# Performance work log

Hardware: AMD Instinct MI355X
Metric: run time of the kernel (lower is better)

The kernel has to match this reference:

```python
import jax, jax.numpy as jnp
from jax import lax
import numpy as np
import math

D = 256; H = 4; DH = 64; PERIOD = 30; WIN = 4; L = 2
AUDIO = 768; MOTION = 33
B = 8; T = 1024; S = 1024


def _pe_table(t, d=D, period=PERIOD):
    pos = np.arange(period, dtype=np.float32)[:, None]
    div = np.exp(np.arange(0, d, 2, dtype=np.float32) * (-math.log(10000.0) / d))
    pe = np.zeros((period, d), np.float32)
    pe[:, 0::2] = np.sin(pos * div)
    pe[:, 1::2] = np.cos(pos * div)
    reps = t // period + 1
    return jnp.asarray(np.tile(pe, (reps, 1))[:t])


def _tgt_mask(t):
    # ALiBi-style bias (quantized by period) + causal mask, per head. [H,t,t]
    slopes = jnp.array([0.25 ** (i + 1) for i in range(H)], jnp.float32)
    i = jnp.arange(t)[:, None]
    j = jnp.arange(t)[None, :]
    rel = i - j
    alibi = jnp.where(rel >= 0, -(rel // PERIOD).astype(jnp.float32), 0.0)
    causal = jnp.where(rel >= 0, 0.0, -jnp.inf)
    return slopes[:, None, None] * alibi + causal[None]


def _mem_mask(t, s):
    i = jnp.arange(t)[:, None]
    j = jnp.arange(s)[None, :]
    return jnp.where(jnp.abs(i - j) <= WIN, 0.0, -jnp.inf)


def _ln(x, g, b, eps=1e-5):
    mu = jnp.mean(x, -1, keepdims=True)
    var = jnp.mean(jnp.square(x - mu), -1, keepdims=True)
    return (x - mu) * lax.rsqrt(var + eps) * g + b


def _mha(xq, xkv, in_w, in_b, out_w, out_b, mask):
    wq, wk, wv = jnp.split(in_w, 3, axis=0)
    bq, bk, bv = jnp.split(in_b, 3)
    q = xq @ wq.T + bq
    k = xkv @ wk.T + bk
    v = xkv @ wv.T + bv
    b_, t_, _ = q.shape
    s_ = k.shape[1]
    q = q.reshape(b_, t_, H, DH)
    k = k.reshape(b_, s_, H, DH)
    v = v.reshape(b_, s_, H, DH)
    scores = jnp.einsum('bthd,bshd->bhts', q, k) / math.sqrt(DH) + mask
    a = jax.nn.softmax(scores, axis=-1)
    o = jnp.einsum('bhts,bshd->bthd', a, v).reshape(b_, t_, D)
    return o @ out_w.T + out_b


def _conv1d(x_nch, w, b):
    y = lax.conv_general_dilated(x_nch, w, (1,), [(2, 2)],
                                 dimension_numbers=('NCH', 'OIH', 'NCH'))
    return y + b[None, :, None]


def setup_inputs() -> dict:
    key = jax.random.key(0)
    ks = iter(jax.random.split(key, 40))

    def r(shape, s=0.05):
        return jax.random.normal(next(ks), shape, jnp.float32) * s

    return {
        'hidden_states': jax.random.normal(next(ks), (B, S, AUDIO), jnp.float32),
        'target_motions': jax.random.uniform(next(ks), (B, T, MOTION), jnp.float32),
        'W_af': r((D, AUDIO)), 'b_af': r((D,)),
        'conv1_w': r((D, D, 5)), 'conv1_b': r((D,)),
        'conv2_w': r((D, D, 5)), 'conv2_b': r((D,)),
        'W_vm': r((D, MOTION)), 'b_vm': r((D,)),
        'sa_in_w': r((L, 3 * D, D)), 'sa_in_b': r((L, 3 * D)),
        'sa_out_w': r((L, D, D)), 'sa_out_b': r((L, D)),
        'ca_in_w': r((L, 3 * D, D)), 'ca_in_b': r((L, 3 * D)),
        'ca_out_w': r((L, D, D)), 'ca_out_b': r((L, D)),
        'ln1_g': jnp.ones((L, D)), 'ln1_b': jnp.zeros((L, D)),
        'ln2_g': jnp.ones((L, D)), 'ln2_b': jnp.zeros((L, D)),
        'ln3_g': jnp.ones((L, D)), 'ln3_b': jnp.zeros((L, D)),
        'ff1_w': r((L, 2 * D, D)), 'ff1_b': r((L, 2 * D)),
        'ff2_w': r((L, D, 2 * D)), 'ff2_b': r((L, D)),
        'W_vr': r((MOTION, D)), 'b_vr': r((MOTION,)),
    }


def reference(hidden_states, target_motions, W_af, b_af, conv1_w, conv1_b,
              conv2_w, conv2_b, W_vm, b_vm, sa_in_w, sa_in_b, sa_out_w,
              sa_out_b, ca_in_w, ca_in_b, ca_out_w, ca_out_b, ln1_g, ln1_b,
              ln2_g, ln2_b, ln3_g, ln3_b, ff1_w, ff1_b, ff2_w, ff2_b,
              W_vr, b_vr):
    # audio encoder: linear + residual temporal convs (exact GELU)
    audio = hidden_states @ W_af.T + b_af                       # [B,S,D]
    c = _conv1d(audio.transpose(0, 2, 1), conv1_w, conv1_b)
    c = jax.nn.gelu(c, approximate=False)
    c = _conv1d(c, conv2_w, conv2_b)
    audio = audio + c.transpose(0, 2, 1)

    b_, t_, _ = target_motions.shape
    motion_in = jnp.concatenate(
        [jnp.zeros((b_, 1, MOTION), target_motions.dtype),
         target_motions[:, :-1]], axis=1)
    x = motion_in @ W_vm.T + b_vm + _pe_table(t_)               # PPE (eval: no dropout)

    tm = _tgt_mask(t_)                                          # [H,t,t]
    mm = _mem_mask(t_, audio.shape[1])                          # [t,s]

    for l in range(L):  # post-norm TransformerDecoderLayer, relu FFN
        x = _ln(x + _mha(x, x, sa_in_w[l], sa_in_b[l], sa_out_w[l], sa_out_b[l], tm),
                ln1_g[l], ln1_b[l])
        x = _ln(x + _mha(x, audio, ca_in_w[l], ca_in_b[l], ca_out_w[l], ca_out_b[l], mm),
                ln2_g[l], ln2_b[l])
        h = jax.nn.relu(x @ ff1_w[l].T + ff1_b[l]) @ ff2_w[l].T + ff2_b[l]
        x = _ln(x + h, ln3_g[l], ln3_b[l])

    return jnp.clip(x @ W_vr.T + b_vr, 0.0, 1.0)
```

## Files before the change

### kernel.cpp

```cpp
#include <hip/hip_runtime.h>
#include <math.h>

#define B_ 8
#define T_ 1024
#define S_ 1024
#define D_ 256
#define H_ 4
#define DH_ 64
#define AUDIO_ 768
#define MOTION_ 33
#define PERIOD_ 30
#define WIN_ 4
#define M_ (B_ * T_)
#define PART_ (B_ * H_ * T_)

typedef _Float16 half8 __attribute__((ext_vector_type(8)));
typedef _Float16 half4 __attribute__((ext_vector_type(4)));
typedef __attribute__((ext_vector_type(4))) float f32x4;

#define O_AF    0
#define O_SAIN  196608
#define O_SAOUT 589824
#define O_CAIN  720896
#define O_CAOUT 1114112
#define O_FF1   1245184
#define O_FF2   1507328
#define O_CONV1 1769472
#define O_CONV2 2097152
#define O_VR    2424832
#define WH_TOT  2441216
#define HID_TOT 6291456

struct CvtSrc { const float* p[17]; };

__global__ __launch_bounds__(256) void cvt_all(
    CvtSrc s, _Float16* __restrict__ wH, _Float16* __restrict__ hidH) {
  const long i = (long)blockIdx.x * 256 + threadIdx.x;
  if (i >= (long)WH_TOT + HID_TOT) return;
  if (i >= WH_TOT) { const long j = i - WH_TOT; hidH[j] = (_Float16)s.p[15][j]; return; }
  if (i >= O_VR) {
    const long j = i - O_VR, oc = j >> 8, cin = j & 255;
    wH[i] = (oc < MOTION_) ? (_Float16)s.p[16][oc * 256 + cin] : (_Float16)0.f;
    return;
  }
  if (i >= O_CONV2) {
    const long j = i - O_CONV2, oc = j / 1280, r = j % 1280, tap = r >> 8, cin = r & 255;
    wH[i] = (_Float16)s.p[14][(oc * 256 + cin) * 5 + tap]; return;
  }
  if (i >= O_CONV1) {
    const long j = i - O_CONV1, oc = j / 1280, r = j % 1280, tap = r >> 8, cin = r & 255;
    wH[i] = (_Float16)s.p[13][(oc * 256 + cin) * 5 + tap]; return;
  }
  int seg; long base;
  if      (i >= 1638400) { seg = 12; base = 1638400; }
  else if (i >= 1507328) { seg = 11; base = 1507328; }
  else if (i >= 1376256) { seg = 10; base = 1376256; }
  else if (i >= 1245184) { seg = 9;  base = 1245184; }
  else if (i >= 1179648) { seg = 8;  base = 1179648; }
  else if (i >= 1114112) { seg = 7;  base = 1114112; }
  else if (i >= 917504)  { seg = 6;  base = 917504; }
  else if (i >= 720896)  { seg = 5;  base = 720896; }
  else if (i >= 655360)  { seg = 4;  base = 655360; }
  else if (i >= 589824)  { seg = 3;  base = 589824; }
  else if (i >= 393216)  { seg = 2;  base = 393216; }
  else if (i >= 196608)  { seg = 1;  base = 196608; }
  else                   { seg = 0;  base = 0; }
  wH[i] = (_Float16)s.p[seg][i - base];
}

__global__ __launch_bounds__(256) void gemm_h(
    const _Float16* __restrict__ A, const _Float16* __restrict__ W,
    const float* __restrict__ bias, float* __restrict__ Cf,
    _Float16* __restrict__ Ch, int M, int N, int K, int relu) {
  __shared__ _Float16 As[2][64][72];
  __shared__ _Float16 Bs[2][64][72];
  const int tid = threadIdx.x;
  const int wave = tid >> 6, lane = tid & 63;
  const int wr = wave >> 1, wc = wave & 1;
  const int lr16 = lane & 15, kq = lane >> 4;
  const int bm = blockIdx.x, bn = blockIdx.y;
  const int sr = tid >> 2, sq = tid & 3;

  const _Float16* Ap = A + (size_t)(bm * 64 + sr) * K + sq * 8;
  const _Float16* Wp = W + (size_t)(bn * 64 + sr) * K + sq * 8;

  half8 ra0 = *reinterpret_cast<const half8*>(Ap);
  half8 ra1 = *reinterpret_cast<const half8*>(Ap + 32);
  half8 rw0 = *reinterpret_cast<const half8*>(Wp);
  half8 rw1 = *reinterpret_cast<const half8*>(Wp + 32);
  f32x4 acc[2][2] = {};

  *reinterpret_cast<half8*>(&As[0][sr][sq * 8]) = ra0;
  *reinterpret_cast<half8*>(&As[0][sr][32 + sq * 8]) = ra1;
  *reinterpret_cast<half8*>(&Bs[0][sr][sq * 8]) = rw0;
  *reinterpret_cast<half8*>(&Bs[0][sr][32 + sq * 8]) = rw1;
  __syncthreads();

  const int nsteps = K >> 6;
  for (int step = 0; step < nsteps; ++step) {
    const int cur = step & 1;
    const bool more = (step + 1 < nsteps);
    if (more) {
      const int kn = (step + 1) << 6;
      ra0 = *reinterpret_cast<const half8*>(Ap + kn);
      ra1 = *reinterpret_cast<const half8*>(Ap + kn + 32);
      rw0 = *reinterpret_cast<const half8*>(Wp + kn);
      rw1 = *reinterpret_cast<const half8*>(Wp + kn + 32);
    }
    half8 af[2][2], bf[2][2];
#pragma unroll
    for (int m = 0; m < 2; ++m)
#pragma unroll
      for (int s = 0; s < 2; ++s)
        af[m][s] = *reinterpret_cast<const half8*>(
            &As[cur][wr * 32 + m * 16 + lr16][s * 32 + kq * 8]);
#pragma unroll
    for (int n = 0; n < 2; ++n)
#pragma unroll
      for (int s = 0; s < 2; ++s)
        bf[n][s] = *reinterpret_cast<const half8*>(
            &Bs[cur][wc * 32 + n * 16 + lr16][s * 32 + kq * 8]);
#pragma unroll
    for (int m = 0; m < 2; ++m)
#pragma unroll
      for (int n = 0; n < 2; ++n)
#pragma unroll
        for (int s = 0; s < 2; ++s)
          acc[m][n] = __builtin_amdgcn_mfma_f32_16x16x32_f16(af[m][s], bf[n][s], acc[m][n], 0, 0, 0);
    if (more) {
      *reinterpret_cast<half8*>(&As[cur ^ 1][sr][sq * 8]) = ra0;
      *reinterpret_cast<half8*>(&As[cur ^ 1][sr][32 + sq * 8]) = ra1;
      *reinterpret_cast<half8*>(&Bs[cur ^ 1][sr][sq * 8]) = rw0;
      *reinterpret_cast<half8*>(&Bs[cur ^ 1][sr][32 + sq * 8]) = rw1;
      __syncthreads();
    }
  }

#pragma unroll
  for (int m = 0; m < 2; ++m) {
#pragma unroll
    for (int n = 0; n < 2; ++n) {
      const int col = bn * 64 + wc * 32 + n * 16 + lr16;
      const float bv = bias[col];
#pragma unroll
      for (int j = 0; j < 4; ++j) {
        const int row = bm * 64 + wr * 32 + m * 16 + kq * 4 + j;
        float v = acc[m][n][j] + bv;
        if (relu) v = fmaxf(v, 0.f);
        const size_t idx = (size_t)row * N + col;
        if (Cf) Cf[idx] = v;
        if (Ch) Ch[idx] = (_Float16)v;
      }
    }
  }
}

__global__ __launch_bounds__(256) void gemm_ca(
    const _Float16* __restrict__ Aq, const _Float16* __restrict__ Akv,
    const _Float16* __restrict__ W, const float* __restrict__ bias,
    _Float16* __restrict__ Oq, _Float16* __restrict__ Okv) {
  __shared__ _Float16 As[2][64][72];
  __shared__ _Float16 Bs[2][64][72];
  const int tid = threadIdx.x;
  const int wave = tid >> 6, lane = tid & 63;
  const int wr = wave >> 1, wc = wave & 1;
  const int lr16 = lane & 15, kq = lane >> 4;
  const int bm = blockIdx.x, bn = blockIdx.y;
  const int sr = tid >> 2, sq = tid & 3;
  const bool isq = (bn < 4);
  const _Float16* A = isq ? Aq : Akv;
  _Float16* Optr = isq ? Oq : Okv;
  const int Nout = isq ? 256 : 512;
  const int ocol0 = (isq ? bn : bn - 4) * 64;

  const _Float16* Ap = A + (size_t)(bm * 64 + sr) * 256 + sq * 8;
  const _Float16* Wp = W + (size_t)(bn * 64 + sr) * 256 + sq * 8;

  half8 ra0 = *reinterpret_cast<const half8*>(Ap);
  half8 ra1 = *reinterpret_cast<const half8*>(Ap + 32);
  half8 rw0 = *reinterpret_cast<const half8*>(Wp);
  half8 rw1 = *reinterpret_cast<const half8*>(Wp + 32);
  f32x4 acc[2][2] = {};

  *reinterpret_cast<half8*>(&As[0][sr][sq * 8]) = ra0;
  *reinterpret_cast<half8*>(&As[0][sr][32 + sq * 8]) = ra1;
  *reinterpret_cast<half8*>(&Bs[0][sr][sq * 8]) = rw0;
  *reinterpret_cast<half8*>(&Bs[0][sr][32 + sq * 8]) = rw1;
  __syncthreads();

  for (int step = 0; step < 4; ++step) {
    const int cur = step & 1;
    const bool more = (step + 1 < 4);
    if (more) {
      const int kn = (step + 1) << 6;
      ra0 = *reinterpret_cast<const half8*>(Ap + kn);
      ra1 = *reinterpret_cast<const half8*>(Ap + kn + 32);
      rw0 = *reinterpret_cast<const half8*>(Wp + kn);
      rw1 = *reinterpret_cast<const half8*>(Wp + kn + 32);
    }
    half8 af[2][2], bf[2][2];
#pragma unroll
    for (int m = 0; m < 2; ++m)
#pragma unroll
      for (int s = 0; s < 2; ++s)
        af[m][s] = *reinterpret_cast<const half8*>(
            &As[cur][wr * 32 + m * 16 + lr16][s * 32 + kq * 8]);
#pragma unroll
    for (int n = 0; n < 2; ++n)
#pragma unroll
      for (int s = 0; s < 2; ++s)
        bf[n][s] = *reinterpret_cast<const half8*>(
            &Bs[cur][wc * 32 + n * 16 + lr16][s * 32 + kq * 8]);
#pragma unroll
    for (int m = 0; m < 2; ++m)
#pragma unroll
      for (int n = 0; n < 2; ++n)
#pragma unroll
        for (int s = 0; s < 2; ++s)
          acc[m][n] = __builtin_amdgcn_mfma_f32_16x16x32_f16(af[m][s], bf[n][s], acc[m][n], 0, 0, 0);
    if (more) {
      *reinterpret_cast<half8*>(&As[cur ^ 1][sr][sq * 8]) = ra0;
      *reinterpret_cast<half8*>(&As[cur ^ 1][sr][32 + sq * 8]) = ra1;
      *reinterpret_cast<half8*>(&Bs[cur ^ 1][sr][sq * 8]) = rw0;
      *reinterpret_cast<half8*>(&Bs[cur ^ 1][sr][32 + sq * 8]) = rw1;
      __syncthreads();
    }
  }

#pragma unroll
  for (int m = 0; m < 2; ++m) {
#pragma unroll
    for (int n = 0; n < 2; ++n) {
      const int lc = wc * 32 + n * 16 + lr16;
      const float bv = bias[bn * 64 + lc];
#pragma unroll
      for (int j = 0; j < 4; ++j) {
        const int row = bm * 64 + wr * 32 + m * 16 + kq * 4 + j;
        Optr[(size_t)row * Nout + ocol0 + lc] = (_Float16)(acc[m][n][j] + bv);
      }
    }
  }
}

__device__ __forceinline__ half8 conv_ld(const _Float16* Xb, int p, int tap, int cin) {
  const int sp = p + tap - 2;
  if (sp < 0 || sp >= S_) { half8 z = {}; return z; }
  return *reinterpret_cast<const half8*>(Xb + (size_t)sp * D_ + cin);
}

__global__ __launch_bounds__(256) void conv_h(
    const _Float16* __restrict__ Xh, const _Float16* __restrict__ Wc,
    const float* __restrict__ bias, _Float16* OutH,
    const _Float16* ResH, int mode) {
  __shared__ _Float16 As[2][64][72];
  __shared__ _Float16 Bs[2][64][72];
  const int tid = threadIdx.x;
  const int wave = tid >> 6, lane = tid & 63;
  const int wr = wave >> 1, wc = wave & 1;
  const int lr16 = lane & 15, kq = lane >> 4;
  const int b = blockIdx.x >> 4;
  const int s0 = (blockIdx.x & 15) * 64;
  const int o0 = blockIdx.y * 64;
  const int sr = tid >> 2, sq = tid & 3;

  const _Float16* Xb = Xh + (size_t)b * S_ * D_;
  const _Float16* Wp = Wc + (size_t)(o0 + sr) * 1280 + sq * 8;
  const int p = s0 + sr;

  half8 ra0 = conv_ld(Xb, p, 0, sq * 8);
  half8 ra1 = conv_ld(Xb, p, 0, 32 + sq * 8);
  half8 rw0 = *reinterpret_cast<const half8*>(Wp);
  half8 rw1 = *reinterpret_cast<const half8*>(Wp + 32);
  f32x4 acc[2][2] = {};

  *reinterpret_cast<half8*>(&As[0][sr][sq * 8]) = ra0;
  *reinterpret_cast<half8*>(&As[0][sr][32 + sq * 8]) = ra1;
  *reinterpret_cast<half8*>(&Bs[0][sr][sq * 8]) = rw0;
  *reinterpret_cast<half8*>(&Bs[0][sr][32 + sq * 8]) = rw1;
  __syncthreads();

  for (int step = 0; step < 20; ++step) {
    const int cur = step & 1;
    const bool more = (step + 1 < 20);
    if (more) {
      const int kn = (step + 1) << 6;
      const int tap = kn >> 8, cb = kn & 255;
      ra0 = conv_ld(Xb, p, tap, cb + sq * 8);
      ra1 = conv_ld(Xb, p, tap, cb + 32 + sq * 8);
      rw0 = *reinterpret_cast<const half8*>(Wp + kn);
      rw1 = *reinterpret_cast<const half8*>(Wp + kn + 32);
    }
    half8 af[2][2], bf[2][2];
#pragma unroll
    for (int m = 0; m < 2; ++m)
#pragma unroll
      for (int s = 0; s < 2; ++s)
        af[m][s] = *reinterpret_cast<const half8*>(
            &As[cur][wr * 32 + m * 16 + lr16][s * 32 + kq * 8]);
#pragma unroll
    for (int n = 0; n < 2; ++n)
#pragma unroll
      for (int s = 0; s < 2; ++s)
        bf[n][s] = *reinterpret_cast<const half8*>(
            &Bs[cur][wc * 32 + n * 16 + lr16][s * 32 + kq * 8]);
#pragma unroll
    for (int m = 0; m < 2; ++m)
#pragma unroll
      for (int n = 0; n < 2; ++n)
#pragma unroll
        for (int s = 0; s < 2; ++s)
          acc[m][n] = __builtin_amdgcn_mfma_f32_16x16x32_f16(af[m][s], bf[n][s], acc[m][n], 0, 0, 0);
    if (more) {
      *reinterpret_cast<half8*>(&As[cur ^ 1][sr][sq * 8]) = ra0;
      *reinterpret_cast<half8*>(&As[cur ^ 1][sr][32 + sq * 8]) = ra1;
      *reinterpret_cast<half8*>(&Bs[cur ^ 1][sr][sq * 8]) = rw0;
      *reinterpret_cast<half8*>(&Bs[cur ^ 1][sr][32 + sq * 8]) = rw1;
      __syncthreads();
    }
  }

#pragma unroll
  for (int m = 0; m < 2; ++m) {
#pragma unroll
    for (int n = 0; n < 2; ++n) {
      const int oc = o0 + wc * 32 + n * 16 + lr16;
      const float bv = bias[oc];
#pragma unroll
      for (int j = 0; j < 4; ++j) {
        const int s = s0 + wr * 32 + m * 16 + kq * 4 + j;
        const size_t idx = ((size_t)b * S_ + s) * D_ + oc;
        float v = acc[m][n][j] + bv;
        if (mode == 0) {
          v = 0.5f * v * (1.f + erff(v * 0.70710678118654752f));
        } else {
          v += (float)ResH[idx];
        }
        OutH[idx] = (_Float16)v;
      }
    }
  }
}

__global__ __launch_bounds__(256) void head_mfma(
    const _Float16* __restrict__ Xh, const _Float16* __restrict__ Wh,
    const float* __restrict__ bv, float* __restrict__ Out) {
  __shared__ _Float16 As[2][64][72];
  __shared__ _Float16 Bs[2][64][72];
  const int tid = threadIdx.x;
  const int wave = tid >> 6, lane = tid & 63;
  const int wr = wave >> 1, wc = wave & 1;
  const int lr16 = lane & 15, kq = lane >> 4;
  const int bm = blockIdx.x;
  const int sr = tid >> 2, sq = tid & 3;

  const _Float16* Ap = Xh + (size_t)(bm * 64 + sr) * D_ + sq * 8;
  const _Float16* Wp = Wh + (size_t)sr * D_ + sq * 8;

  half8 ra0 = *reinterpret_cast<const half8*>(Ap);
  half8 ra1 = *reinterpret_cast<const half8*>(Ap + 32);
  half8 rw0 = *reinterpret_cast<const half8*>(Wp);
  half8 rw1 = *reinterpret_cast<const half8*>(Wp + 32);
  f32x4 acc[2][2] = {};

  *reinterpret_cast<half8*>(&As[0][sr][sq * 8]) = ra0;
  *reinterpret_cast<half8*>(&As[0][sr][32 + sq * 8]) = ra1;
  *reinterpret_cast<half8*>(&Bs[0][sr][sq * 8]) = rw0;
  *reinterpret_cast<half8*>(&Bs[0][sr][32 + sq * 8]) = rw1;
  __syncthreads();

  for (int step = 0; step < 4; ++step) {
    const int cur = step & 1;
    const bool more = (step + 1 < 4);
    if (more) {
      const int kn = (step + 1) << 6;
      ra0 = *reinterpret_cast<const half8*>(Ap + kn);
      ra1 = *reinterpret_cast<const half8*>(Ap + kn + 32);
      rw0 = *reinterpret_cast<const half8*>(Wp + kn);
      rw1 = *reinterpret_cast<const half8*>(Wp + kn + 32);
    }
    half8 af[2][2], bf[2][2];
#pragma unroll
    for (int m = 0; m < 2; ++m)
#pragma unroll
      for (int s = 0; s < 2; ++s)
        af[m][s] = *reinterpret_cast<const half8*>(
            &As[cur][wr * 32 + m * 16 + lr16][s * 32 + kq * 8]);
#pragma unroll
    for (int n = 0; n < 2; ++n)
#pragma unroll
      for (int s = 0; s < 2; ++s)
        bf[n][s] = *reinterpret_cast<const half8*>(
            &Bs[cur][wc * 32 + n * 16 + lr16][s * 32 + kq * 8]);
#pragma unroll
    for (int m = 0; m < 2; ++m)
#pragma unroll
      for (int n = 0; n < 2; ++n)
#pragma unroll
        for (int s = 0; s < 2; ++s)
          acc[m][n] = __builtin_amdgcn_mfma_f32_16x16x32_f16(af[m][s], bf[n][s], acc[m][n], 0, 0, 0);
    if (more) {
      *reinterpret_cast<half8*>(&As[cur ^ 1][sr][sq * 8]) = ra0;
      *reinterpret_cast<half8*>(&As[cur ^ 1][sr][32 + sq * 8]) = ra1;
      *reinterpret_cast<half8*>(&Bs[cur ^ 1][sr][sq * 8]) = rw0;
      *reinterpret_cast<half8*>(&Bs[cur ^ 1][sr][32 + sq * 8]) = rw1;
      __syncthreads();
    }
  }

#pragma unroll
  for (int m = 0; m < 2; ++m) {
#pragma unroll
    for (int n = 0; n < 2; ++n) {
      const int col = wc * 32 + n * 16 + lr16;
      if (col < MOTION_) {
        const float bb = bv[col];
#pragma unroll
        for (int j = 0; j < 4; ++j) {
          const int row = bm * 64 + wr * 32 + m * 16 + kq * 4 + j;
          float v = acc[m][n][j] + bb;
          Out[(size_t)row * MOTION_ + col] = fminf(fmaxf(v, 0.f), 1.f);
        }
      }
    }
  }
}

__global__ __launch_bounds__(256) void motion_pe(
    const float* __restrict__ TM, const float* __restrict__ Wvm,
    const float* __restrict__ bvm, float* __restrict__ Xout,
    _Float16* __restrict__ XoutH) {
  const int d = threadIdx.x;
  const int bt = blockIdx.x;
  const int t = bt & (T_ - 1);
  const int b = bt >> 10;
  float acc = bvm[d];
  if (t > 0) {
    const float* mrow = TM + ((size_t)b * T_ + t - 1) * MOTION_;
    const float* wrow = Wvm + (size_t)d * MOTION_;
#pragma unroll
    for (int m = 0; m < MOTION_; ++m) acc += mrow[m] * wrow[m];
  }
  const int pos = t % PERIOD_;
  const int i2 = d >> 1;
  const float div = expf((float)(2 * i2) * (-9.210340371976184f / 256.f));
  const float ang = (float)pos * div;
  acc += (d & 1) ? cosf(ang) : sinf(ang);
  Xout[(size_t)bt * D_ + d] = acc;
  XoutH[(size_t)bt * D_ + d] = (_Float16)acc;
}

#define RSK_ 72
#define RSV_ 64
__global__ __launch_bounds__(512) void self_attn(
    const _Float16* __restrict__ QKV, float* __restrict__ Opart,
    float* __restrict__ Ml, float* __restrict__ Ll) {
  __shared__ _Float16 Ks[2][64 * RSK_];
  __shared__ _Float16 VTs[2][64 * RSV_];
  __shared__ _Float16 Ps[8][16 * RSK_];
  const int qtb = blockIdx.x >> 1, half = blockIdx.x & 1;
  const int h = blockIdx.y, b = blockIdx.z;
  const int tid = threadIdx.x;
  const int wave = tid >> 6, lane = tid & 63;
  const int lo = lane & 15, hi = lane >> 4;
  const float slope = exp2f(-2.f * (float)(h + 1));
  const int qloc = wave * 16 + lo;
  const int tq = qtb * 128 + qloc;
  const size_t base = (size_t)b * T_ * 768 + h * 64;
  const int sj = tid >> 3, sch = tid & 7;

  half8 qf[2];
#pragma unroll
  for (int s = 0; s < 2; ++s)
    qf[s] = *reinterpret_cast<const half8*>(
        QKV + base + (size_t)(qtb * 128 + qloc) * 768 + s * 32 + hi * 8);

  f32x4 oacc[4] = {};
  float mrun = -1e30f, lrun = 0.f;

  const int nloc = qtb + 1;
  const int kt0 = half * nloc;

  half8 rk, rv;
  {
    const size_t rowoff = base + (size_t)(kt0 * 64 + sj) * 768;
    rk = *reinterpret_cast<const half8*>(QKV + rowoff + 256 + sch * 8);
    rv = *reinterpret_cast<const half8*>(QKV + rowoff + 512 + sch * 8);
    *reinterpret_cast<half8*>(&Ks[0][sj * RSK_ + sch * 8]) = rk;
#pragma unroll
    for (int r = 0; r < 8; ++r) {
      const int d = sch * 8 + r;
      const int sw = ((d & 7) ^ (d >> 3)) << 3;
      VTs[0][d * RSV_ + (sj ^ sw)] = rv[r];
    }
  }
  __syncthreads();

  for (int i = 0; i < nloc; ++i) {
    const int kt = kt0 + i;
    const int cur = i & 1;
    const bool more = (i + 1 < nloc);
    if (more) {
      const size_t rowoff = base + (size_t)((kt + 1) * 64 + sj) * 768;
      rk = *reinterpret_cast<const half8*>(QKV + rowoff + 256 + sch * 8);
      rv = *reinterpret_cast<const half8*>(QKV + rowoff + 512 + sch * 8);
    }

    f32x4 st[4] = {};
    __builtin_amdgcn_s_setprio(1);
#pragma unroll
    for (int f = 0; f < 4; ++f) {
#pragma unroll
      for (int s = 0; s < 2; ++s) {
        const half8 kf = *reinterpret_cast<const half8*>(
            &Ks[cur][(f * 16 + lo) * RSK_ + s * 32 + hi * 8]);
        st[f] = __builtin_amdgcn_mfma_f32_16x16x32_f16(kf, qf[s], st[f], 0, 0, 0);
      }
    }
    __builtin_amdgcn_s_setprio(0);

    float sc[4][4];
    float tmax = -1e30f;
#pragma unroll
    for (int f = 0; f < 4; ++f)
#pragma unroll
      for (int r = 0; r < 4; ++r) {
        const int j = kt * 64 + f * 16 + hi * 4 + r;
        const int rel = tq - j;
        const float v = (rel >= 0)
            ? st[f][r] * 0.125f - slope * (float)(rel / PERIOD_) : -1e30f;
        sc[f][r] = v;
        tmax = fmaxf(tmax, v);
      }
    tmax = fmaxf(tmax, __shfl_xor(tmax, 16, 64));
    tmax = fmaxf(tmax, __shfl_xor(tmax, 32, 64));
    const float mnew = fmaxf(fmaxf(mrun, tmax), -1e20f);
    const float scale = __expf(mrun - mnew);

    float psum = 0.f;
#pragma unroll
    for (int f = 0; f < 4; ++f) {
      half4 ph;
#pragma unroll
      for (int r = 0; r < 4; ++r) {
        const float pv = __expf(sc[f][r] - mnew);
        psum += pv;
        ph[r] = (_Float16)pv;
      }
      *reinterpret_cast<half4*>(&Ps[wave][lo * RSK_ + f * 16 + hi * 4]) = ph;
    }
    psum += __shfl_xor(psum, 16, 64);
    psum += __shfl_xor(psum, 32, 64);
    lrun = lrun * scale + psum;
    mrun = mnew;

    float rsc[4];
#pragma unroll
    for (int r = 0; r < 4; ++r) rsc[r] = __shfl(scale, hi * 4 + r, 64);
#pragma unroll
    for (int nf = 0; nf < 4; ++nf)
#pragma unroll
      for (int r = 0; r < 4; ++r) oacc[nf][r] *= rsc[r];

    __builtin_amdgcn_s_setprio(1);
#pragma unroll
    for (int s = 0; s < 2; ++s) {
      const half8 pf = *reinterpret_cast<const half8*>(
          &Ps[wave][lo * RSK_ + s * 32 + hi * 8]);
#pragma unroll
      for (int nf = 0; nf < 4; ++nf) {
        const int d = nf * 16 + lo;
        const int sw = ((d & 7) ^ (d >> 3)) << 3;
        const half8 vf = *reinterpret_cast<const half8*>(
            &VTs[cur][d * RSV_ + ((s * 32 + hi * 8) ^ sw)]);
        oacc[nf] = __builtin_amdgcn_mfma_f32_16x16x32_f16(pf, vf, oacc[nf], 0, 0, 0);
      }
    }
    __builtin_amdgcn_s_setprio(0);

    if (more) {
      *reinterpret_cast<half8*>(&Ks[cur ^ 1][sj * RSK_ + sch * 8]) = rk;
#pragma unroll
      for (int r = 0; r < 8; ++r) {
        const int d = sch * 8 + r;
        const int sw = ((d & 7) ^ (d >> 3)) << 3;
        VTs[cur ^ 1][d * RSV_ + (sj ^ sw)] = rv[r];
      }
      __syncthreads();
    }
  }

  const size_t rbase = ((size_t)b * H_ + h) * T_;
  const size_t hoff = (size_t)half * PART_;
#pragma unroll
  for (int nf = 0; nf < 4; ++nf)
#pragma unroll
    for (int r = 0; r < 4; ++r) {
      const int q = qtb * 128 + wave * 16 + hi * 4 + r;
      Opart[(hoff + rbase + q) * 64 + nf * 16 + lo] = oacc[nf][r];
    }
  if (hi == 0) {
    const int q = qtb * 128 + wave * 16 + lo;
    Ml[hoff + rbase + q] = mrun;
    Ll[hoff + rbase + q] = lrun;
  }
}

__global__ __launch_bounds__(256) void attn_merge(
    const float* __restrict__ Opart, const float* __restrict__ Ml,
    const float* __restrict__ Ll, _Float16* __restrict__ O) {
  const int tid = threadIdx.x;
  const int d = tid & 63;
  const long row = (long)blockIdx.x * 4 + (tid >> 6);
  const float m0 = Ml[row], m1 = Ml[PART_ + row];
  const float l0 = Ll[row], l1 = Ll[PART_ + row];
  const float m = fmaxf(m0, m1);
  const float w0 = __expf(m0 - m), w1 = __expf(m1 - m);
  const float inv = 1.f / (l0 * w0 + l1 * w1);
  const float o = (Opart[row * 64 + d] * w0 +
                   Opart[(long)PART_ * 64 + row * 64 + d] * w1) * inv;
  const int b = (int)(row >> 12);
  const int h = (int)((row >> 10) & 3);
  const int t = (int)(row & (T_ - 1));
  O[(((size_t)b * T_ + t) * D_) + h * 64 + d] = (_Float16)o;
}

__global__ __launch_bounds__(128) void cross_attn(
    const _Float16* __restrict__ Q, const _Float16* __restrict__ KV,
    _Float16* __restrict__ O) {
  const int gid = blockIdx.x * 128 + threadIdx.x;
  const int h = gid & 3;
  const int bt = gid >> 2;
  const int t = bt & (T_ - 1);
  const int b = bt >> 10;

  float q[64];
  const _Float16* qp = Q + (size_t)bt * D_ + h * 64;
#pragma unroll
  for (int d0 = 0; d0 < 64; d0 += 8) {
    const half8 v = *reinterpret_cast<const half8*>(qp + d0);
#pragma unroll
    for (int e = 0; e < 8; ++e) q[d0 + e] = (float)v[e];
  }

  const int j0 = (t - WIN_ > 0) ? t - WIN_ : 0;
  const int j1 = (t + WIN_ < S_ - 1) ? t + WIN_ : S_ - 1;
  const int nj = j1 - j0 + 1;

  float sc[9];
  float mx = -1e30f;
#pragma unroll
  for (int jj = 0; jj < 9; ++jj) {
    if (jj < nj) {
      const _Float16* kp = KV + ((size_t)b * S_ + j0 + jj) * 512 + h * 64;
      float s = 0.f;
#pragma unroll
      for (int d0 = 0; d0 < 64; d0 += 8) {
        const half8 kv = *reinterpret_cast<const half8*>(kp + d0);
#pragma unroll
        for (int e = 0; e < 8; ++e) s += q[d0 + e] * (float)kv[e];
      }
      sc[jj] = s * 0.125f;
      mx = fmaxf(mx, sc[jj]);
    } else {
      sc[jj] = -1e30f;
    }
  }
  float l = 0.f;
  float p[9];
#pragma unroll
  for (int jj = 0; jj < 9; ++jj) { p[jj] = __expf(sc[jj] - mx); l += p[jj]; }
  const float inv = 1.f / l;

  float o[64];
#pragma unroll
  for (int d = 0; d < 64; ++d) o[d] = 0.f;
#pragma unroll
  for (int jj = 0; jj < 9; ++jj) {
    if (jj < nj) {
      const float pj = p[jj] * inv;
      const _Float16* vp = KV + ((size_t)b * S_ + j0 + jj) * 512 + 256 + h * 64;
#pragma unroll
      for (int d0 = 0; d0 < 64; d0 += 8) {
        const half8 vv = *reinterpret_cast<const half8*>(vp + d0);
#pragma unroll
        for (int e = 0; e < 8; ++e) o[d0 + e] += pj * (float)vv[e];
      }
    }
  }
  _Float16* op = O + (size_t)bt * D_ + h * 64;
#pragma unroll
  for (int d = 0; d < 64; ++d) op[d] = (_Float16)o[d];
}

__global__ __launch_bounds__(256) void ln_res(
    const float* X, const _Float16* __restrict__ R,
    const float* __restrict__ g, const float* __restrict__ bta,
    float* Out, _Float16* __restrict__ OutH) {
  const int wid = threadIdx.x >> 6, lane = threadIdx.x & 63;
  const size_t row = (size_t)blockIdx.x * 4 + wid;
  const float* xp = X + row * D_;
  const _Float16* rp = R + row * D_;
  float v[4];
  float s = 0.f;
#pragma unroll
  for (int k = 0; k < 4; ++k) {
    const int d = lane + k * 64;
    v[k] = xp[d] + (float)rp[d];
    s += v[k];
  }
#pragma unroll
  for (int off = 32; off; off >>= 1) s += __shfl_xor(s, off, 64);
  const float mu = s * (1.f / 256.f);
  float var = 0.f;
#pragma unroll
  for (int k = 0; k < 4; ++k) { const float d = v[k] - mu; var += d * d; }
#pragma unroll
  for (int off = 32; off; off >>= 1) var += __shfl_xor(var, off, 64);
  const float rs = rsqrtf(var * (1.f / 256.f) + 1e-5f);
#pragma unroll
  for (int k = 0; k < 4; ++k) {
    const int d = lane + k * 64;
    const float o = (v[k] - mu) * rs * g[d] + bta[d];
    Out[row * D_ + d] = o;
    OutH[row * D_ + d] = (_Float16)o;
  }
}

extern "C" void kernel_launch(void* const* d_in, const int* in_sizes, int n_in,
                              void* d_out, int out_size, void* d_ws, size_t ws_size,
                              hipStream_t stream) {
  (void)in_sizes; (void)n_in; (void)out_size; (void)ws_size;
  const float* hidden = (const float*)d_in[0];
  const float* tmot   = (const float*)d_in[1];
  const float* W_af   = (const float*)d_in[2];
  const float* b_af   = (const float*)d_in[3];
  const float* c1w    = (const float*)d_in[4];
  const float* c1b    = (const float*)d_in[5];
  const float* c2w    = (const float*)d_in[6];
  const float* c2b    = (const float*)d_in[7];
  const float* Wvm    = (const float*)d_in[8];
  const float* bvm    = (const float*)d_in[9];
  const float* sa_in_w  = (const float*)d_in[10];
  const float* sa_in_b  = (const float*)d_in[11];
  const float* sa_out_w = (const float*)d_in[12];
  const float* sa_out_b = (const float*)d_in[13];
  const float* ca_in_w  = (const float*)d_in[14];
  const float* ca_in_b  = (const float*)d_in[15];
  const float* ca_out_w = (const float*)d_in[16];
  const float* ca_out_b = (const float*)d_in[17];
  const float* ln1g = (const float*)d_in[18];
  const float* ln1b = (const float*)d_in[19];
  const float* ln2g = (const float*)d_in[20];
  const float* ln2b = (const float*)d_in[21];
  const float* ln3g = (const float*)d_in[22];
  const float* ln3b = (const float*)d_in[23];
  const float* ff1w = (const float*)d_in[24];
  const float* ff1b = (const float*)d_in[25];
  const float* ff2w = (const float*)d_in[26];
  const float* ff2b = (const float*)d_in[27];
  const float* Wvr  = (const float*)d_in[28];
  const float* bvr  = (const float*)d_in[29];
  float* out = (float*)d_out;

  float* ws = (float*)d_ws;
  const size_t BSD = (size_t)M_ * D_;
  float* x     = ws + BSD;
  _Float16* t1h = (_Float16*)(ws + 2 * BSD);
  _Float16* hb = (_Float16*)(ws + 3 * BSD);
  _Float16* Rh      = hb;
  _Float16* x_h     = hb + 3 * BSD;
  _Float16* audio_h = hb + 4 * BSD;
  _Float16* att_h   = hb + 5 * BSD;
  _Float16* wH      = hb + 6 * BSD;
  _Float16* ckv_h   = Rh + BSD;
  float* Opart = (float*)(wH + WH_TOT);
  float* Ml    = Opart + (size_t)2 * PART_ * 64;
  float* Ll    = Ml + (size_t)2 * PART_;

  const dim3 blk(256);

  CvtSrc cs;
  cs.p[0] = W_af;
  cs.p[1] = sa_in_w;            cs.p[2] = sa_in_w + 768 * 256;
  cs.p[3] = sa_out_w;           cs.p[4] = sa_out_w + 256 * 256;
  cs.p[5] = ca_in_w;            cs.p[6] = ca_in_w + 768 * 256;
  cs.p[7] = ca_out_w;           cs.p[8] = ca_out_w + 256 * 256;
  cs.p[9] = ff1w;               cs.p[10] = ff1w + 512 * 256;
  cs.p[11] = ff2w;              cs.p[12] = ff2w + 256 * 512;
  cs.p[13] = c1w;               cs.p[14] = c2w;
  cs.p[15] = hidden;            cs.p[16] = Wvr;
  cvt_all<<<dim3((WH_TOT + HID_TOT + 255) / 256), blk, 0, stream>>>(cs, wH, Rh);

  gemm_h<<<dim3(M_ / 64, 4), blk, 0, stream>>>(Rh, wH + O_AF, b_af, nullptr, audio_h,
                                               M_, 256, 768, 0);
  conv_h<<<dim3(128, 4), blk, 0, stream>>>(audio_h, wH + O_CONV1, c1b, t1h, nullptr, 0);
  conv_h<<<dim3(128, 4), blk, 0, stream>>>(t1h, wH + O_CONV2, c2b, audio_h, audio_h, 1);

  motion_pe<<<dim3(M_), blk, 0, stream>>>(tmot, Wvm, bvm, x, x_h);

  for (int l = 0; l < 2; ++l) {
    gemm_h<<<dim3(M_ / 64, 12), blk, 0, stream>>>(
        x_h, wH + O_SAIN + l * 196608, sa_in_b + l * 768, nullptr, Rh, M_, 768, 256, 0);
    self_attn<<<dim3(T_ / 128 * 2, H_, B_), dim3(512), 0, stream>>>(Rh, Opart, Ml, Ll);
    attn_merge<<<dim3(PART_ / 4), blk, 0, stream>>>(Opart, Ml, Ll, att_h);
    gemm_h<<<dim3(M_ / 64, 4), blk, 0, stream>>>(
        att_h, wH + O_SAOUT + l * 65536, sa_out_b + l * 256, nullptr, t1h, M_, 256, 256, 0);
    ln_res<<<dim3(M_ / 4), blk, 0, stream>>>(x, t1h, ln1g + l * 256, ln1b + l * 256, x, x_h);

    gemm_ca<<<dim3(M_ / 64, 12), blk, 0, stream>>>(
        x_h, audio_h, wH + O_CAIN + l * 196608, ca_in_b + l * 768, Rh, ckv_h);
    cross_attn<<<dim3(M_ * H_ / 128), dim3(128), 0, stream>>>(Rh, ckv_h, att_h);
    gemm_h<<<dim3(M_ / 64, 4), blk, 0, stream>>>(
        att_h, wH + O_CAOUT + l * 65536, ca_out_b + l * 256, nullptr, t1h, M_, 256, 256, 0);
    ln_res<<<dim3(M_ / 4), blk, 0, stream>>>(x, t1h, ln2g + l * 256, ln2b + l * 256, x, x_h);

    gemm_h<<<dim3(M_ / 64, 8), blk, 0, stream>>>(
        x_h, wH + O_FF1 + l * 131072, ff1b + l * 512, nullptr, Rh, M_, 512, 256, 1);
    gemm_h<<<dim3(M_ / 64, 4), blk, 0, stream>>>(
        Rh, wH + O_FF2 + l * 131072, ff2b + l * 256, nullptr, t1h, M_, 256, 512, 0);
    ln_res<<<dim3(M_ / 4), blk, 0, stream>>>(x, t1h, ln3g + l * 256, ln3b + l * 256, x, x_h);
  }

  head_mfma<<<dim3(M_ / 64), blk, 0, stream>>>(x_h, wH + O_VR, bvr, out);
}
```

Before: 332.9 us.

## Fuse fp32-to-fp16 input conversion into audio GEMM and attention merge into out-proj GEMM

The audio feature projection GEMM now reads the fp32 hidden states directly and converts them to fp16 while staging tiles into shared memory, so the conversion kernel no longer writes an fp16 copy. The self-attention split-KV merge kernel is removed; the output-projection GEMM instead loads both partial outputs plus their max/sum statistics and combines them while building its A tiles. This removes one kernel launch per layer and the global round trips of the intermediate fp16 buffers. In exchange, the GEMMs read more bytes per tile (fp32 inputs, two partials) and the merge work is repeated across the four N-blocks.

After: 315.8 us (median of 2 runs). 5.2% less time.

```diff
diff --git a/kernel.cpp b/kernel.cpp
--- a/kernel.cpp
+++ b/kernel.cpp
@@ -29,15 +29,13 @@
 #define O_CONV2 2097152
 #define O_VR    2424832
 #define WH_TOT  2441216
-#define HID_TOT 6291456
 
 struct CvtSrc { const float* p[17]; };
 
 __global__ __launch_bounds__(256) void cvt_all(
-    CvtSrc s, _Float16* __restrict__ wH, _Float16* __restrict__ hidH) {
+    CvtSrc s, _Float16* __restrict__ wH) {
   const long i = (long)blockIdx.x * 256 + threadIdx.x;
-  if (i >= (long)WH_TOT + HID_TOT) return;
-  if (i >= WH_TOT) { const long j = i - WH_TOT; hidH[j] = (_Float16)s.p[15][j]; return; }
+  if (i >= WH_TOT) return;
   if (i >= O_VR) {
     const long j = i - O_VR, oc = j >> 8, cin = j & 255;
     wH[i] = (oc < MOTION_) ? (_Float16)s.p[16][oc * 256 + cin] : (_Float16)0.f;
@@ -150,6 +148,234 @@
         const size_t idx = (size_t)row * N + col;
         if (Cf) Cf[idx] = v;
         if (Ch) Ch[idx] = (_Float16)v;
+      }
+    }
+  }
+}
+
+__global__ __launch_bounds__(256) void gemm_af(
+    const float* __restrict__ A, const _Float16* __restrict__ W,
+    const float* __restrict__ bias, _Float16* __restrict__ Ch,
+    int M, int N, int K) {
+  __shared__ _Float16 As[2][64][72];
+  __shared__ _Float16 Bs[2][64][72];
+  const int tid = threadIdx.x;
+  const int wave = tid >> 6, lane = tid & 63;
+  const int wr = wave >> 1, wc = wave & 1;
+  const int lr16 = lane & 15, kq = lane >> 4;
+  const int bm = blockIdx.x, bn = blockIdx.y;
+  const int sr = tid >> 2, sq = tid & 3;
+
+  const float* Ap = A + (size_t)(bm * 64 + sr) * K + sq * 8;
+  const _Float16* Wp = W + (size_t)(bn * 64 + sr) * K + sq * 8;
+
+  float4 fa0, fa1, fa2, fa3;
+  half8 rw0, rw1;
+  fa0 = *reinterpret_cast<const float4*>(Ap);
+  fa1 = *reinterpret_cast<const float4*>(Ap + 4);
+  fa2 = *reinterpret_cast<const float4*>(Ap + 32);
+  fa3 = *reinterpret_cast<const float4*>(Ap + 36);
+  rw0 = *reinterpret_cast<const half8*>(Wp);
+  rw1 = *reinterpret_cast<const half8*>(Wp + 32);
+  f32x4 acc[2][2] = {};
+
+  {
+    half8 pa0, pa1;
+    pa0[0] = (_Float16)fa0.x; pa0[1] = (_Float16)fa0.y; pa0[2] = (_Float16)fa0.z; pa0[3] = (_Float16)fa0.w;
+    pa0[4] = (_Float16)fa1.x; pa0[5] = (_Float16)fa1.y; pa0[6] = (_Float16)fa1.z; pa0[7] = (_Float16)fa1.w;
+    pa1[0] = (_Float16)fa2.x; pa1[1] = (_Float16)fa2.y; pa1[2] = (_Float16)fa2.z; pa1[3] = (_Float16)fa2.w;
+    pa1[4] = (_Float16)fa3.x; pa1[5] = (_Float16)fa3.y; pa1[6] = (_Float16)fa3.z; pa1[7] = (_Float16)fa3.w;
+    *reinterpret_cast<half8*>(&As[0][sr][sq * 8]) = pa0;
+    *reinterpret_cast<half8*>(&As[0][sr][32 + sq * 8]) = pa1;
+    *reinterpret_cast<half8*>(&Bs[0][sr][sq * 8]) = rw0;
+    *reinterpret_cast<half8*>(&Bs[0][sr][32 + sq * 8]) = rw1;
+  }
+  __syncthreads();
+
+  const int nsteps = K >> 6;
+  for (int step = 0; step < nsteps; ++step) {
+    const int cur = step & 1;
+    const bool more = (step + 1 < nsteps);
+    if (more) {
+      const int kn = (step + 1) << 6;
+      fa0 = *reinterpret_cast<const float4*>(Ap + kn);
+      fa1 = *reinterpret_cast<const float4*>(Ap + kn + 4);
+      fa2 = *reinterpret_cast<const float4*>(Ap + kn + 32);
+      fa3 = *reinterpret_cast<const float4*>(Ap + kn + 36);
+      rw0 = *reinterpret_cast<const half8*>(Wp + kn);
+      rw1 = *reinterpret_cast<const half8*>(Wp + kn + 32);
+    }
+    half8 af[2][2], bf[2][2];
+#pragma unroll
+    for (int m = 0; m < 2; ++m)
+#pragma unroll
+      for (int s = 0; s < 2; ++s)
+        af[m][s] = *reinterpret_cast<const half8*>(
+            &As[cur][wr * 32 + m * 16 + lr16][s * 32 + kq * 8]);
+#pragma unroll
+    for (int n = 0; n < 2; ++n)
+#pragma unroll
+      for (int s = 0; s < 2; ++s)
+        bf[n][s] = *reinterpret_cast<const half8*>(
+            &Bs[cur][wc * 32 + n * 16 + lr16][s * 32 + kq * 8]);
+#pragma unroll
+    for (int m = 0; m < 2; ++m)
+#pragma unroll
+      for (int n = 0; n < 2; ++n)
+#pragma unroll
+        for (int s = 0; s < 2; ++s)
+          acc[m][n] = __builtin_amdgcn_mfma_f32_16x16x32_f16(af[m][s], bf[n][s], acc[m][n], 0, 0, 0);
+    if (more) {
+      half8 pa0, pa1;
+      pa0[0] = (_Float16)fa0.x; pa0[1] = (_Float16)fa0.y; pa0[2] = (_Float16)fa0.z; pa0[3] = (_Float16)fa0.w;
+      pa0[4] = (_Float16)fa1.x; pa0[5] = (_Float16)fa1.y; pa0[6] = (_Float16)fa1.z; pa0[7] = (_Float16)fa1.w;
+      pa1[0] = (_Float16)fa2.x; pa1[1] = (_Float16)fa2.y; pa1[2] = (_Float16)fa2.z; pa1[3] = (_Float16)fa2.w;
+      pa1[4] = (_Float16)fa3.x; pa1[5] = (_Float16)fa3.y; pa1[6] = (_Float16)fa3.z; pa1[7] = (_Float16)fa3.w;
+      *reinterpret_cast<half8*>(&As[cur ^ 1][sr][sq * 8]) = pa0;
+      *reinterpret_cast<half8*>(&As[cur ^ 1][sr][32 + sq * 8]) = pa1;
+      *reinterpret_cast<half8*>(&Bs[cur ^ 1][sr][sq * 8]) = rw0;
+      *reinterpret_cast<half8*>(&Bs[cur ^ 1][sr][32 + sq * 8]) = rw1;
+      __syncthreads();
+    }
+  }
+
+#pragma unroll
+  for (int m = 0; m < 2; ++m) {
+#pragma unroll
+    for (int n = 0; n < 2; ++n) {
+      const int col = bn * 64 + wc * 32 + n * 16 + lr16;
+      const float bv = bias[col];
+#pragma unroll
+      for (int j = 0; j < 4; ++j) {
+        const int row = bm * 64 + wr * 32 + m * 16 + kq * 4 + j;
+        Ch[(size_t)row * N + col] = (_Float16)(acc[m][n][j] + bv);
+      }
+    }
+  }
+}
+
+struct SaPre {
+  float4 h0a, h0b, h0c, h0d;
+  float4 h1a, h1b, h1c, h1d;
+  float m0, m1, l0, l1;
+};
+
+__device__ __forceinline__ SaPre sa_load(
+    const float* __restrict__ Opart, const float* __restrict__ Ml,
+    const float* __restrict__ Ll, size_t p, int sq) {
+  SaPre x;
+  const float* o0 = Opart + p * 64;
+  const float* o1 = Opart + (size_t)PART_ * 64 + p * 64;
+  x.h0a = *reinterpret_cast<const float4*>(o0 + sq * 8);
+  x.h0b = *reinterpret_cast<const float4*>(o0 + sq * 8 + 4);
+  x.h0c = *reinterpret_cast<const float4*>(o0 + 32 + sq * 8);
+  x.h0d = *reinterpret_cast<const float4*>(o0 + 36 + sq * 8);
+  x.h1a = *reinterpret_cast<const float4*>(o1 + sq * 8);
+  x.h1b = *reinterpret_cast<const float4*>(o1 + sq * 8 + 4);
+  x.h1c = *reinterpret_cast<const float4*>(o1 + 32 + sq * 8);
+  x.h1d = *reinterpret_cast<const float4*>(o1 + 36 + sq * 8);
+  x.m0 = Ml[p]; x.m1 = Ml[(size_t)PART_ + p];
+  x.l0 = Ll[p]; x.l1 = Ll[(size_t)PART_ + p];
+  return x;
+}
+
+__device__ __forceinline__ void sa_write(
+    _Float16* dst0, _Float16* dst1, const SaPre& x) {
+  const float m = fmaxf(x.m0, x.m1);
+  const float w0 = __expf(x.m0 - m), w1 = __expf(x.m1 - m);
+  const float inv = 1.f / (x.l0 * w0 + x.l1 * w1);
+  const float g0h0[8] = {x.h0a.x, x.h0a.y, x.h0a.z, x.h0a.w,
+                         x.h0b.x, x.h0b.y, x.h0b.z, x.h0b.w};
+  const float g0h1[8] = {x.h1a.x, x.h1a.y, x.h1a.z, x.h1a.w,
+                         x.h1b.x, x.h1b.y, x.h1b.z, x.h1b.w};
+  const float g1h0[8] = {x.h0c.x, x.h0c.y, x.h0c.z, x.h0c.w,
+                         x.h0d.x, x.h0d.y, x.h0d.z, x.h0d.w};
+  const float g1h1[8] = {x.h1c.x, x.h1c.y, x.h1c.z, x.h1c.w,
+                         x.h1d.x, x.h1d.y, x.h1d.z, x.h1d.w};
+  half8 pa, pb;
+#pragma unroll
+  for (int e = 0; e < 8; ++e) {
+    pa[e] = (_Float16)((g0h0[e] * w0 + g0h1[e] * w1) * inv);
+    pb[e] = (_Float16)((g1h0[e] * w0 + g1h1[e] * w1) * inv);
+  }
+  *reinterpret_cast<half8*>(dst0) = pa;
+  *reinterpret_cast<half8*>(dst1) = pb;
+}
+
+__global__ __launch_bounds__(256) void gemm_sa(
+    const float* __restrict__ Opart, const float* __restrict__ Ml,
+    const float* __restrict__ Ll, const _Float16* __restrict__ W,
+    const float* __restrict__ bias, _Float16* __restrict__ Ch) {
+  __shared__ _Float16 As[2][64][72];
+  __shared__ _Float16 Bs[2][64][72];
+  const int tid = threadIdx.x;
+  const int wave = tid >> 6, lane = tid & 63;
+  const int wr = wave >> 1, wc = wave & 1;
+  const int lr16 = lane & 15, kq = lane >> 4;
+  const int bm = blockIdx.x, bn = blockIdx.y;
+  const int sr = tid >> 2, sq = tid & 3;
+
+  const int r = bm * 64 + sr;
+  const size_t pb0 = (size_t)(r >> 10) * 4096 + (r & 1023);
+  const _Float16* Wp = W + (size_t)(bn * 64 + sr) * 256 + sq * 8;
+
+  SaPre ax = sa_load(Opart, Ml, Ll, pb0, sq);
+  half8 rw0 = *reinterpret_cast<const half8*>(Wp);
+  half8 rw1 = *reinterpret_cast<const half8*>(Wp + 32);
+  f32x4 acc[2][2] = {};
+
+  sa_write(&As[0][sr][sq * 8], &As[0][sr][32 + sq * 8], ax);
+  *reinterpret_cast<half8*>(&Bs[0][sr][sq * 8]) = rw0;
+  *reinterpret_cast<half8*>(&Bs[0][sr][32 + sq * 8]) = rw1;
+  __syncthreads();
+
+  for (int step = 0; step < 4; ++step) {
+    const int cur = step & 1;
+    const bool more = (step + 1 < 4);
+    if (more) {
+      ax = sa_load(Opart, Ml, Ll, pb0 + (size_t)(step + 1) * 1024, sq);
+      const int kn = (step + 1) << 6;
+      rw0 = *reinterpret_cast<const half8*>(Wp + kn);
+      rw1 = *reinterpret_cast<const half8*>(Wp + kn + 32);
+    }
+    half8 af[2][2], bf[2][2];
+#pragma unroll
+    for (int m = 0; m < 2; ++m)
+#pragma unroll
+      for (int s = 0; s < 2; ++s)
+        af[m][s] = *reinterpret_cast<const half8*>(
+            &As[cur][wr * 32 + m * 16 + lr16][s * 32 + kq * 8]);
+#pragma unroll
+    for (int n = 0; n < 2; ++n)
+#pragma unroll
+      for (int s = 0; s < 2; ++s)
+        bf[n][s] = *reinterpret_cast<const half8*>(
+            &Bs[cur][wc * 32 + n * 16 + lr16][s * 32 + kq * 8]);
+#pragma unroll
+    for (int m = 0; m < 2; ++m)
+#pragma unroll
+      for (int n = 0; n < 2; ++n)
+#pragma unroll
+        for (int s = 0; s < 2; ++s)
+          acc[m][n] = __builtin_amdgcn_mfma_f32_16x16x32_f16(af[m][s], bf[n][s], acc[m][n], 0, 0, 0);
+    if (more) {
+      sa_write(&As[cur ^ 1][sr][sq * 8], &As[cur ^ 1][sr][32 + sq * 8], ax);
+      *reinterpret_cast<half8*>(&Bs[cur ^ 1][sr][sq * 8]) = rw0;
+      *reinterpret_cast<half8*>(&Bs[cur ^ 1][sr][32 + sq * 8]) = rw1;
+      __syncthreads();
+    }
+  }
+
+#pragma unroll
+  for (int m = 0; m < 2; ++m) {
+#pragma unroll
+    for (int n = 0; n < 2; ++n) {
+      const int col = bn * 64 + wc * 32 + n * 16 + lr16;
+      const float bv = bias[col];
+#pragma unroll
+      for (int j = 0; j < 4; ++j) {
+        const int row = bm * 64 + wr * 32 + m * 16 + kq * 4 + j;
+        Ch[(size_t)row * 256 + col] = (_Float16)(acc[m][n][j] + bv);
       }
     }
   }
@@ -603,25 +829,6 @@
     Ml[hoff + rbase + q] = mrun;
     Ll[hoff + rbase + q] = lrun;
   }
-}
-
-__global__ __launch_bounds__(256) void attn_merge(
-    const float* __restrict__ Opart, const float* __restrict__ Ml,
-    const float* __restrict__ Ll, _Float16* __restrict__ O) {
-  const int tid = threadIdx.x;
-  const int d = tid & 63;
-  const long row = (long)blockIdx.x * 4 + (tid >> 6);
-  const float m0 = Ml[row], m1 = Ml[PART_ + row];
-  const float l0 = Ll[row], l1 = Ll[PART_ + row];
-  const float m = fmaxf(m0, m1);
-  const float w0 = __expf(m0 - m), w1 = __expf(m1 - m);
-  const float inv = 1.f / (l0 * w0 + l1 * w1);
-  const float o = (Opart[row * 64 + d] * w0 +
-                   Opart[(long)PART_ * 64 + row * 64 + d] * w1) * inv;
-  const int b = (int)(row >> 12);
-  const int h = (int)((row >> 10) & 3);
-  const int t = (int)(row & (T_ - 1));
-  O[(((size_t)b * T_ + t) * D_) + h * 64 + d] = (_Float16)o;
 }
 
 __global__ __launch_bounds__(128) void cross_attn(
@@ -789,10 +996,10 @@
   cs.p[11] = ff2w;              cs.p[12] = ff2w + 256 * 512;
   cs.p[13] = c1w;               cs.p[14] = c2w;
   cs.p[15] = hidden;            cs.p[16] = Wvr;
-  cvt_all<<<dim3((WH_TOT + HID_TOT + 255) / 256), blk, 0, stream>>>(cs, wH, Rh);
-
-  gemm_h<<<dim3(M_ / 64, 4), blk, 0, stream>>>(Rh, wH + O_AF, b_af, nullptr, audio_h,
-                                               M_, 256, 768, 0);
+  cvt_all<<<dim3(WH_TOT / 256), blk, 0, stream>>>(cs, wH);
+
+  gemm_af<<<dim3(M_ / 64, 4), blk, 0, stream>>>(hidden, wH + O_AF, b_af, audio_h,
+                                                M_, 256, 768);
   conv_h<<<dim3(128, 4), blk, 0, stream>>>(audio_h, wH + O_CONV1, c1b, t1h, nullptr, 0);
   conv_h<<<dim3(128, 4), blk, 0, stream>>>(t1h, wH + O_CONV2, c2b, audio_h, audio_h, 1);
 
@@ -802,9 +1009,8 @@
     gemm_h<<<dim3(M_ / 64, 12), blk, 0, stream>>>(
         x_h, wH + O_SAIN + l * 196608, sa_in_b + l * 768, nullptr, Rh, M_, 768, 256, 0);
     self_attn<<<dim3(T_ / 128 * 2, H_, B_), dim3(512), 0, stream>>>(Rh, Opart, Ml, Ll);
-    attn_merge<<<dim3(PART_ / 4), blk, 0, stream>>>(Opart, Ml, Ll, att_h);
-    gemm_h<<<dim3(M_ / 64, 4), blk, 0, stream>>>(
-        att_h, wH + O_SAOUT + l * 65536, sa_out_b + l * 256, nullptr, t1h, M_, 256, 256, 0);
+    gemm_sa<<<dim3(M_ / 64, 4), blk, 0, stream>>>(
+        Opart, Ml, Ll, wH + O_SAOUT + l * 65536, sa_out_b + l * 256, t1h);
     ln_res<<<dim3(M_ / 4), blk, 0, stream>>>(x, t1h, ln1g + l * 256, ln1b + l * 256, x, x_h);
 
     gemm_ca<<<dim3(M_ / 64, 12), blk, 0, stream>>>(
```
